# Optimization experiments

Hardware: AMD Instinct MI355X
Metric: run time of the kernel (lower is better)

The kernel has to match this reference:

```python
import jax, jax.numpy as jnp
import numpy as np


def shift_2d(x, H, W):
    # x: (B, T=H*W, C); quarter-channel directional shifts (gamma=1/4), C must be divisible by 4
    B, T, C = x.shape
    g = C // 4
    xi = x.reshape(B, H, W, C)
    # group 0: shift right along W (output[..., 1:, :] = input[..., :-1, :])
    s0 = jnp.pad(xi[:, :, : W - 1, 0:g], ((0, 0), (0, 0), (1, 0), (0, 0)))
    # group 1: shift left along W
    s1 = jnp.pad(xi[:, :, 1:, g : 2 * g], ((0, 0), (0, 0), (0, 1), (0, 0)))
    # group 2: shift down along H
    s2 = jnp.pad(xi[:, : H - 1, :, 2 * g : 3 * g], ((0, 0), (1, 0), (0, 0), (0, 0)))
    # group 3: shift up along H
    s3 = jnp.pad(xi[:, 1:, :, 3 * g : 4 * g], ((0, 0), (0, 1), (0, 0), (0, 0)))
    out = jnp.concatenate([s0, s1, s2, s3], axis=-1)  # C == 4*g here
    return out.reshape(B, T, C)


def wkv(w, u, k, v):
    # RWKV v4 WKV recurrence with running-max numerical stabilization.
    # w, u: (C,) ; k, v: (B, T, C) ; returns y: (B, T, C)
    B, T, C = k.shape
    NEG = jnp.float32(-1e38)

    def step(carry, kv):
        p, q, o = carry  # numerator state, denominator state, running log-max
        kt, vt = kv
        no = jnp.maximum(o, u + kt)
        A = jnp.exp(o - no)
        Bc = jnp.exp(u + kt - no)
        y = (A * p + Bc * vt) / (A * q + Bc)
        no2 = jnp.maximum(w + o, kt)
        A2 = jnp.exp(w + o - no2)
        B2 = jnp.exp(kt - no2)
        return (A2 * p + B2 * vt, A2 * q + B2, no2), y

    init = (jnp.zeros((B, C), k.dtype), jnp.zeros((B, C), k.dtype), jnp.full((B, C), NEG, k.dtype))
    kT = jnp.moveaxis(k, 1, 0)
    vT = jnp.moveaxis(v, 1, 0)
    _, yT = jax.lax.scan(step, init, (kT, vT))
    return jnp.moveaxis(yT, 0, 1)


def setup_inputs() -> dict:
    key = jax.random.key(0)
    ks = jax.random.split(key, 7)
    B, H, W, C = 16, 96, 96, 192
    T = H * W
    x = jax.random.normal(ks[0], (B, T, C), jnp.float32)
    Wk = jax.random.normal(ks[1], (C, C), jnp.float32) * 0.02
    Wv = jax.random.normal(ks[2], (C, C), jnp.float32) * 0.02
    Wr = jax.random.normal(ks[3], (C, C), jnp.float32) * 0.02
    Wo = jax.random.normal(ks[4], (C, C), jnp.float32) * 0.02
    spatial_decay = jax.random.normal(ks[5], (3, C), jnp.float32)
    spatial_first = jax.random.normal(ks[6], (3, C), jnp.float32)
    return {"x": x, "Wk": Wk, "Wv": Wv, "Wr": Wr, "Wo": Wo,
            "spatial_decay": spatial_decay, "spatial_first": spatial_first,
            "H": H, "W": W}


def reference(x, Wk, Wv, Wr, Wo, spatial_decay, spatial_first, H, W):
    B, T, C = x.shape
    xs = shift_2d(x, H, W)
    k = xs @ Wk.T
    v = xs @ Wv.T
    sr = jax.nn.sigmoid(xs @ Wr.T)
    w = spatial_decay[0] / T
    u = spatial_first[0] / T
    y = wkv(w, u, k, v)
    return (sr * y) @ Wo.T
```

## Files before the change

kernel.cpp:

```cpp
#include <hip/hip_runtime.h>
#include <hip/hip_bf16.h>

typedef __bf16 bf16x8 __attribute__((ext_vector_type(8)));
typedef float f32x4 __attribute__((ext_vector_type(4)));

using bf = __hip_bfloat16;

constexpr int cB = 16, cH = 96, cW = 96, cC = 192;
constexpr int cT = cH * cW;
constexpr int cM = cB * cT;
constexpr int CH = 96;
constexpr int NS = cT / CH;
constexpr float Tinv = 1.0f / 9216.0f;

__device__ __forceinline__ int swz(int row, int bytecol) {
    return row * 384 + (bytecol ^ ((row & 7) << 4));
}
__device__ __forceinline__ float bflo(unsigned u) { return __uint_as_float(u << 16); }
__device__ __forceinline__ float bfhi(unsigned u) { return __uint_as_float(u & 0xffff0000u); }

__global__ __launch_bounds__(256) void convw_k(
    const float* __restrict__ Wk, const float* __restrict__ Wv,
    const float* __restrict__ Wr, const float* __restrict__ Wo,
    bf* __restrict__ out)
{
    int i = (blockIdx.x * 256 + threadIdx.x) * 8;
    int mat = i / 36864, off = i % 36864;
    const float* s = mat == 0 ? Wk : (mat == 1 ? Wv : (mat == 2 ? Wr : Wo));
    const float4* sp = reinterpret_cast<const float4*>(s + off);
    float4 a0 = sp[0], a1 = sp[1];
    bf16x8 pk;
    pk[0]=(__bf16)a0.x; pk[1]=(__bf16)a0.y; pk[2]=(__bf16)a0.z; pk[3]=(__bf16)a0.w;
    pk[4]=(__bf16)a1.x; pk[5]=(__bf16)a1.y; pk[6]=(__bf16)a1.z; pk[7]=(__bf16)a1.w;
    *reinterpret_cast<bf16x8*>(reinterpret_cast<__bf16*>(out) + i) = pk;
}

template <int MODE>
__global__ __launch_bounds__(512, 2) void gemm_k(
    const void* __restrict__ Ap, const bf* __restrict__ Wb,
    void* __restrict__ O0, void* __restrict__ O1, void* __restrict__ O2)
{
    constexpr int NMAT = (MODE == 0) ? 3 : 1;
    __shared__ char lds[2 * 64 * 384 + 192 * 384];
    const int tid = threadIdx.x, bx = blockIdx.x;
    const int lane = tid & 63, wid = tid >> 6;
    const int wm = wid >> 2, wn = wid & 3;
    const int lr = lane & 15, lq = lane >> 4;

    int rj[3], kbj[3];
#pragma unroll
    for (int j = 0; j < 3; ++j) { int idx = tid + j * 512; rj[j] = idx / 24; kbj[j] = idx % 24; }

    float4 pf[6];
    int4   pi[3];

    for (int mat = 0; mat < NMAT; ++mat) {
        {
            const bf* Wt = Wb + (size_t)mat * 192 * cC;
            char* Bb = &lds[0] + 2 * 64 * 384;
            for (int it = 0; it < 9; ++it) {
                int idx = tid + it * 512;
                int r = idx / 24, kb = idx % 24;
                int4 val = *reinterpret_cast<const int4*>(Wt + r * cC + kb * 8);
                *reinterpret_cast<int4*>(Bb + swz(r, kb * 16)) = val;
            }
        }
        if constexpr (MODE == 0) {
            const float* Af = (const float*)Ap;
#pragma unroll
            for (int j = 0; j < 3; ++j) {
                int gm = bx * 64 + rj[j];
                int b = gm / cT, t = gm % cT, h = t / cW, w = t % cW;
                int grp = kbj[j] / 6;
                int hs = h + (grp == 2 ? -1 : (grp == 3 ? 1 : 0));
                int ws2 = w + (grp == 0 ? -1 : (grp == 1 ? 1 : 0));
                pf[2*j] = float4{0,0,0,0}; pf[2*j+1] = float4{0,0,0,0};
                if (hs >= 0 && hs < cH && ws2 >= 0 && ws2 < cW) {
                    const float4* s = reinterpret_cast<const float4*>(
                        Af + ((size_t)b * cT + (size_t)hs * cW + ws2) * cC + kbj[j] * 8);
                    pf[2*j] = s[0]; pf[2*j+1] = s[1];
                }
            }
#pragma unroll
            for (int j = 0; j < 3; ++j) {
                bf16x8 pk;
                pk[0]=(__bf16)pf[2*j].x; pk[1]=(__bf16)pf[2*j].y; pk[2]=(__bf16)pf[2*j].z; pk[3]=(__bf16)pf[2*j].w;
                pk[4]=(__bf16)pf[2*j+1].x; pk[5]=(__bf16)pf[2*j+1].y; pk[6]=(__bf16)pf[2*j+1].z; pk[7]=(__bf16)pf[2*j+1].w;
                *reinterpret_cast<bf16x8*>(&lds[0] + swz(rj[j], kbj[j] * 16)) = pk;
            }
        } else {
            const bf* Az = (const bf*)Ap;
#pragma unroll
            for (int j = 0; j < 3; ++j)
                pi[j] = *reinterpret_cast<const int4*>(Az + (size_t)(bx * 64 + rj[j]) * cC + kbj[j] * 8);
#pragma unroll
            for (int j = 0; j < 3; ++j)
                *reinterpret_cast<int4*>(&lds[0] + swz(rj[j], kbj[j] * 16)) = pi[j];
        }
        __syncthreads();

        for (int i = 0; i < 9; ++i) {
            const int tix = bx + 256 * i;
            if (i < 8) {
                const int tn = bx + 256 * (i + 1);
                if constexpr (MODE == 0) {
                    const float* Af = (const float*)Ap;
#pragma unroll
                    for (int j = 0; j < 3; ++j) {
                        int gm = tn * 64 + rj[j];
                        int b = gm / cT, t = gm % cT, h = t / cW, w = t % cW;
                        int grp = kbj[j] / 6;
                        int hs = h + (grp == 2 ? -1 : (grp == 3 ? 1 : 0));
                        int ws2 = w + (grp == 0 ? -1 : (grp == 1 ? 1 : 0));
                        pf[2*j] = float4{0,0,0,0}; pf[2*j+1] = float4{0,0,0,0};
                        if (hs >= 0 && hs < cH && ws2 >= 0 && ws2 < cW) {
                            const float4* s = reinterpret_cast<const float4*>(
                                Af + ((size_t)b * cT + (size_t)hs * cW + ws2) * cC + kbj[j] * 8);
                            pf[2*j] = s[0]; pf[2*j+1] = s[1];
                        }
                    }
                } else {
                    const bf* Az = (const bf*)Ap;
#pragma unroll
                    for (int j = 0; j < 3; ++j)
                        pi[j] = *reinterpret_cast<const int4*>(Az + (size_t)(tn * 64 + rj[j]) * cC + kbj[j] * 8);
                }
            }
            char* Ab = &lds[0] + (i & 1) * (64 * 384);
            char* Bb = &lds[0] + 2 * 64 * 384;
            f32x4 acc[2][3] = {};
#pragma unroll
            for (int kk = 0; kk < 6; ++kk) {
                const int bc = kk * 64 + lq * 16;
                bf16x8 af[2], bfr[3];
#pragma unroll
                for (int mt = 0; mt < 2; ++mt)
                    af[mt] = *reinterpret_cast<const bf16x8*>(Ab + swz(wm * 32 + mt * 16 + lr, bc));
#pragma unroll
                for (int nt = 0; nt < 3; ++nt)
                    bfr[nt] = *reinterpret_cast<const bf16x8*>(Bb + swz(wn * 48 + nt * 16 + lr, bc));
#pragma unroll
                for (int mt = 0; mt < 2; ++mt)
#pragma unroll
                    for (int nt = 0; nt < 3; ++nt)
                        acc[mt][nt] = __builtin_amdgcn_mfma_f32_16x16x32_bf16(
                            af[mt], bfr[nt], acc[mt][nt], 0, 0, 0);
            }
            if constexpr (MODE == 0) {
                bf* Os = (bf*)(mat == 0 ? O0 : (mat == 1 ? O1 : O2));
#pragma unroll
                for (int mt = 0; mt < 2; ++mt)
#pragma unroll
                    for (int nt = 0; nt < 3; ++nt)
#pragma unroll
                        for (int j = 0; j < 4; ++j) {
                            int row = tix * 64 + wm * 32 + mt * 16 + lq * 4 + j;
                            int col = wn * 48 + nt * 16 + lr;
                            float v = acc[mt][nt][j];
                            if (mat == 2) v = 1.0f / (1.0f + __expf(-v));
                            Os[(size_t)row * cC + col] = __float2bfloat16(v);
                        }
            } else {
                float* Os = (float*)O0;
#pragma unroll
                for (int mt = 0; mt < 2; ++mt)
#pragma unroll
                    for (int nt = 0; nt < 3; ++nt)
#pragma unroll
                        for (int j = 0; j < 4; ++j) {
                            int row = tix * 64 + wm * 32 + mt * 16 + lq * 4 + j;
                            int col = wn * 48 + nt * 16 + lr;
                            Os[(size_t)row * cC + col] = acc[mt][nt][j];
                        }
            }
            if (i < 8) {
                char* An = &lds[0] + ((i + 1) & 1) * (64 * 384);
                if constexpr (MODE == 0) {
#pragma unroll
                    for (int j = 0; j < 3; ++j) {
                        bf16x8 pk;
                        pk[0]=(__bf16)pf[2*j].x; pk[1]=(__bf16)pf[2*j].y; pk[2]=(__bf16)pf[2*j].z; pk[3]=(__bf16)pf[2*j].w;
                        pk[4]=(__bf16)pf[2*j+1].x; pk[5]=(__bf16)pf[2*j+1].y; pk[6]=(__bf16)pf[2*j+1].z; pk[7]=(__bf16)pf[2*j+1].w;
                        *reinterpret_cast<bf16x8*>(An + swz(rj[j], kbj[j] * 16)) = pk;
                    }
                } else {
#pragma unroll
                    for (int j = 0; j < 3; ++j)
                        *reinterpret_cast<int4*>(An + swz(rj[j], kbj[j] * 16)) = pi[j];
                }
            }
            __syncthreads();
        }
    }
}

__global__ __launch_bounds__(192) void wkv_pass1(
    const bf* __restrict__ k, const bf* __restrict__ v,
    const float* __restrict__ sd,
    float* __restrict__ stP, float* __restrict__ stQ, float* __restrict__ stO)
{
    const int c2 = threadIdx.x % 96, sub = threadIdx.x / 96;
    const int b = blockIdx.y, ch = blockIdx.x * 2 + sub;
    const int c0 = c2 * 2;
    const float w0 = sd[c0] * Tinv, w1 = sd[c0 + 1] * Tinv;
    size_t base = ((size_t)b * cT + (size_t)ch * CH) * cC + c0;
    float p0 = 0.f, q0 = 0.f, o0 = -1e38f;
    float p1 = 0.f, q1 = 0.f, o1 = -1e38f;
    for (int s = 0; s < CH; ++s) {
        unsigned kw = *reinterpret_cast<const unsigned*>(k + base + (size_t)s * cC);
        unsigned vw = *reinterpret_cast<const unsigned*>(v + base + (size_t)s * cC);
        float kt0 = bflo(kw), kt1 = bfhi(kw);
        float vt0 = bflo(vw), vt1 = bfhi(vw);
        float no0 = fmaxf(w0 + o0, kt0);
        float A0 = __expf(w0 + o0 - no0), B0 = __expf(kt0 - no0);
        p0 = A0 * p0 + B0 * vt0; q0 = A0 * q0 + B0; o0 = no0;
        float no1 = fmaxf(w1 + o1, kt1);
        float A1 = __expf(w1 + o1 - no1), B1 = __expf(kt1 - no1);
        p1 = A1 * p1 + B1 * vt1; q1 = A1 * q1 + B1; o1 = no1;
    }
    size_t si = ((size_t)b * NS + ch) * cC + c0;
    *reinterpret_cast<float2*>(stP + si) = make_float2(p0, p1);
    *reinterpret_cast<float2*>(stQ + si) = make_float2(q0, q1);
    *reinterpret_cast<float2*>(stO + si) = make_float2(o0, o1);
}

__global__ __launch_bounds__(192) void wkv_pass2(
    const float* __restrict__ stP, const float* __restrict__ stQ,
    const float* __restrict__ stO, const float* __restrict__ sd,
    float* __restrict__ iP, float* __restrict__ iQ, float* __restrict__ iO)
{
    const int c = threadIdx.x, b = blockIdx.x;
    const float w = sd[c] * Tinv;
    const float Lw = w * (float)CH;
    float p = 0.f, q = 0.f, o = -1e38f;
    size_t si = (size_t)b * NS * cC + c;
    float sp = stP[si], sq = stQ[si], so = stO[si];
    for (int ch = 0; ch < NS; ++ch) {
        float np_ = 0.f, nq_ = 0.f, no_ = -1e38f;
        if (ch + 1 < NS) {
            size_t sj = si + (size_t)(ch + 1) * cC;
            np_ = stP[sj]; nq_ = stQ[sj]; no_ = stO[sj];
        }
        size_t sc = si + (size_t)ch * cC;
        iP[sc] = p; iQ[sc] = q; iO[sc] = o;
        float po = o + Lw;
        float m = fmaxf(po, so);
        float e1 = __expf(po - m), e2 = __expf(so - m);
        p = e1 * p + e2 * sp;
        q = e1 * q + e2 * sq;
        o = m;
        sp = np_; sq = nq_; so = no_;
    }
}

__global__ __launch_bounds__(192) void wkv_pass3(
    const bf* __restrict__ k, const bf* __restrict__ v, const bf* __restrict__ sr,
    const float* __restrict__ sd, const float* __restrict__ sf,
    const float* __restrict__ iP, const float* __restrict__ iQ,
    const float* __restrict__ iO, bf* __restrict__ z)
{
    const int c2 = threadIdx.x % 96, sub = threadIdx.x / 96;
    const int b = blockIdx.y, ch = blockIdx.x * 2 + sub;
    const int c0 = c2 * 2;
    const float w0 = sd[c0] * Tinv, w1 = sd[c0 + 1] * Tinv;
    const float u0 = sf[c0] * Tinv, u1 = sf[c0 + 1] * Tinv;
    size_t si = ((size_t)b * NS + ch) * cC + c0;
    float2 pp = *reinterpret_cast<const float2*>(iP + si);
    float2 qq = *reinterpret_cast<const float2*>(iQ + si);
    float2 oo = *reinterpret_cast<const float2*>(iO + si);
    float p0 = pp.x, q0 = qq.x, o0 = oo.x;
    float p1 = pp.y, q1 = qq.y, o1 = oo.y;
    size_t base = ((size_t)b * cT + (size_t)ch * CH) * cC + c0;
    for (int s = 0; s < CH; ++s) {
        size_t ix = base + (size_t)s * cC;
        unsigned kw = *reinterpret_cast<const unsigned*>(k + ix);
        unsigned vw = *reinterpret_cast<const unsigned*>(v + ix);
        unsigned rw = *reinterpret_cast<const unsigned*>(sr + ix);
        float kt0 = bflo(kw), kt1 = bfhi(kw);
        float vt0 = bflo(vw), vt1 = bfhi(vw);
        float rt0 = bflo(rw), rt1 = bfhi(rw);

        float no0 = fmaxf(o0, u0 + kt0);
        float Ae0 = __expf(o0 - no0), Be0 = __expf(u0 + kt0 - no0);
        float y0 = (Ae0 * p0 + Be0 * vt0) / (Ae0 * q0 + Be0);
        float no1 = fmaxf(o1, u1 + kt1);
        float Ae1 = __expf(o1 - no1), Be1 = __expf(u1 + kt1 - no1);
        float y1 = (Ae1 * p1 + Be1 * vt1) / (Ae1 * q1 + Be1);

        bf z0 = __float2bfloat16(rt0 * y0);
        bf z1 = __float2bfloat16(rt1 * y1);
        unsigned zp = (unsigned)*reinterpret_cast<unsigned short*>(&z0)
                    | ((unsigned)*reinterpret_cast<unsigned short*>(&z1) << 16);
        *reinterpret_cast<unsigned*>(z + ix) = zp;

        float m0 = fmaxf(w0 + o0, kt0);
        float A0 = __expf(w0 + o0 - m0), B0 = __expf(kt0 - m0);
        p0 = A0 * p0 + B0 * vt0; q0 = A0 * q0 + B0; o0 = m0;
        float m1 = fmaxf(w1 + o1, kt1);
        float A1 = __expf(w1 + o1 - m1), B1 = __expf(kt1 - m1);
        p1 = A1 * p1 + B1 * vt1; q1 = A1 * q1 + B1; o1 = m1;
    }
}

extern "C" void kernel_launch(void* const* d_in, const int* in_sizes, int n_in,
                              void* d_out, int out_size, void* d_ws, size_t ws_size,
                              hipStream_t stream)
{
    const float* x  = (const float*)d_in[0];
    const float* Wk = (const float*)d_in[1];
    const float* Wv = (const float*)d_in[2];
    const float* Wr = (const float*)d_in[3];
    const float* Wo = (const float*)d_in[4];
    const float* sd = (const float*)d_in[5];
    const float* sf = (const float*)d_in[6];
    float* out = (float*)d_out;

    const size_t nEl = (size_t)cM * cC;
    bf* kbuf  = (bf*)d_out;
    bf* srbuf = (bf*)d_out + nEl;
    char* ws = (char*)d_ws;
    bf* vbuf = (bf*)ws;
    bf* zbuf = (bf*)(ws + 2 * nEl);
    const size_t stN = (size_t)cB * NS * cC;
    float* stP = (float*)(ws + 4 * nEl);
    float* stQ = stP + stN;
    float* stO = stQ + stN;
    float* iP  = stO + stN;
    float* iQ  = iP + stN;
    float* iO  = iQ + stN;
    bf* wbf = (bf*)(iO + stN);

    convw_k<<<dim3(72), dim3(256), 0, stream>>>(Wk, Wv, Wr, Wo, wbf);
    gemm_k<0><<<dim3(256), dim3(512), 0, stream>>>(x, wbf, kbuf, vbuf, srbuf);
    wkv_pass1<<<dim3(NS / 2, cB), dim3(192), 0, stream>>>(kbuf, vbuf, sd, stP, stQ, stO);
    wkv_pass2<<<dim3(cB), dim3(192), 0, stream>>>(stP, stQ, stO, sd, iP, iQ, iO);
    wkv_pass3<<<dim3(NS / 2, cB), dim3(192), 0, stream>>>(
        kbuf, vbuf, srbuf, sd, sf, iP, iQ, iO, zbuf);
    gemm_k<1><<<dim3(256), dim3(512), 0, stream>>>(
        zbuf, wbf + (size_t)576 * cC, out, nullptr, nullptr);
}
```

Measured before the change: 245.1 us.

## Halve WKV chunk length, prefetch next-step k/v/r, and scan chunk states in place

Shrinks the per-chunk length of the chunked WKV scan from 96 to 48 steps. This doubles the number of blocks in passes 1 and 3 and shortens each thread's serial dependency chain. Both per-chunk passes now software-prefetch the next timestep's k, v and r words into registers to hide global-load latency behind the exp math. Pass 2 writes the exclusive-prefix states back over the chunk-state buffers instead of separate arrays, which removes three workspace arrays. The trade-off is that the serial pass 2 now loops over twice as many chunks per batch, using only 16 blocks.

```diff
diff --git a/kernel.cpp b/kernel.cpp
--- a/kernel.cpp
+++ b/kernel.cpp
@@ -9,7 +9,7 @@
 constexpr int cB = 16, cH = 96, cW = 96, cC = 192;
 constexpr int cT = cH * cW;
 constexpr int cM = cB * cT;
-constexpr int CH = 96;
+constexpr int CH = 48;
 constexpr int NS = cT / CH;
 constexpr float Tinv = 1.0f / 9216.0f;
 
@@ -206,17 +206,23 @@
     size_t base = ((size_t)b * cT + (size_t)ch * CH) * cC + c0;
     float p0 = 0.f, q0 = 0.f, o0 = -1e38f;
     float p1 = 0.f, q1 = 0.f, o1 = -1e38f;
+    unsigned kwc = *reinterpret_cast<const unsigned*>(k + base);
+    unsigned vwc = *reinterpret_cast<const unsigned*>(v + base);
     for (int s = 0; s < CH; ++s) {
-        unsigned kw = *reinterpret_cast<const unsigned*>(k + base + (size_t)s * cC);
-        unsigned vw = *reinterpret_cast<const unsigned*>(v + base + (size_t)s * cC);
-        float kt0 = bflo(kw), kt1 = bfhi(kw);
-        float vt0 = bflo(vw), vt1 = bfhi(vw);
+        unsigned kwn = 0, vwn = 0;
+        if (s + 1 < CH) {
+            kwn = *reinterpret_cast<const unsigned*>(k + base + (size_t)(s + 1) * cC);
+            vwn = *reinterpret_cast<const unsigned*>(v + base + (size_t)(s + 1) * cC);
+        }
+        float kt0 = bflo(kwc), kt1 = bfhi(kwc);
+        float vt0 = bflo(vwc), vt1 = bfhi(vwc);
         float no0 = fmaxf(w0 + o0, kt0);
         float A0 = __expf(w0 + o0 - no0), B0 = __expf(kt0 - no0);
         p0 = A0 * p0 + B0 * vt0; q0 = A0 * q0 + B0; o0 = no0;
         float no1 = fmaxf(w1 + o1, kt1);
         float A1 = __expf(w1 + o1 - no1), B1 = __expf(kt1 - no1);
         p1 = A1 * p1 + B1 * vt1; q1 = A1 * q1 + B1; o1 = no1;
+        kwc = kwn; vwc = vwn;
     }
     size_t si = ((size_t)b * NS + ch) * cC + c0;
     *reinterpret_cast<float2*>(stP + si) = make_float2(p0, p1);
@@ -225,9 +231,8 @@
 }
 
 __global__ __launch_bounds__(192) void wkv_pass2(
-    const float* __restrict__ stP, const float* __restrict__ stQ,
-    const float* __restrict__ stO, const float* __restrict__ sd,
-    float* __restrict__ iP, float* __restrict__ iQ, float* __restrict__ iO)
+    float* __restrict__ stP, float* __restrict__ stQ, float* __restrict__ stO,
+    const float* __restrict__ sd)
 {
     const int c = threadIdx.x, b = blockIdx.x;
     const float w = sd[c] * Tinv;
@@ -242,7 +247,7 @@
             np_ = stP[sj]; nq_ = stQ[sj]; no_ = stO[sj];
         }
         size_t sc = si + (size_t)ch * cC;
-        iP[sc] = p; iQ[sc] = q; iO[sc] = o;
+        stP[sc] = p; stQ[sc] = q; stO[sc] = o;
         float po = o + Lw;
         float m = fmaxf(po, so);
         float e1 = __expf(po - m), e2 = __expf(so - m);
@@ -271,14 +276,20 @@
     float p0 = pp.x, q0 = qq.x, o0 = oo.x;
     float p1 = pp.y, q1 = qq.y, o1 = oo.y;
     size_t base = ((size_t)b * cT + (size_t)ch * CH) * cC + c0;
+    unsigned kwc = *reinterpret_cast<const unsigned*>(k + base);
+    unsigned vwc = *reinterpret_cast<const unsigned*>(v + base);
+    unsigned rwc = *reinterpret_cast<const unsigned*>(sr + base);
     for (int s = 0; s < CH; ++s) {
-        size_t ix = base + (size_t)s * cC;
-        unsigned kw = *reinterpret_cast<const unsigned*>(k + ix);
-        unsigned vw = *reinterpret_cast<const unsigned*>(v + ix);
-        unsigned rw = *reinterpret_cast<const unsigned*>(sr + ix);
-        float kt0 = bflo(kw), kt1 = bfhi(kw);
-        float vt0 = bflo(vw), vt1 = bfhi(vw);
-        float rt0 = bflo(rw), rt1 = bfhi(rw);
+        unsigned kwn = 0, vwn = 0, rwn = 0;
+        if (s + 1 < CH) {
+            size_t nx = base + (size_t)(s + 1) * cC;
+            kwn = *reinterpret_cast<const unsigned*>(k + nx);
+            vwn = *reinterpret_cast<const unsigned*>(v + nx);
+            rwn = *reinterpret_cast<const unsigned*>(sr + nx);
+        }
+        float kt0 = bflo(kwc), kt1 = bfhi(kwc);
+        float vt0 = bflo(vwc), vt1 = bfhi(vwc);
+        float rt0 = bflo(rwc), rt1 = bfhi(rwc);
 
         float no0 = fmaxf(o0, u0 + kt0);
         float Ae0 = __expf(o0 - no0), Be0 = __expf(u0 + kt0 - no0);
@@ -291,7 +302,7 @@
         bf z1 = __float2bfloat16(rt1 * y1);
         unsigned zp = (unsigned)*reinterpret_cast<unsigned short*>(&z0)
                     | ((unsigned)*reinterpret_cast<unsigned short*>(&z1) << 16);
-        *reinterpret_cast<unsigned*>(z + ix) = zp;
+        *reinterpret_cast<unsigned*>(z + base + (size_t)s * cC) = zp;
 
         float m0 = fmaxf(w0 + o0, kt0);
         float A0 = __expf(w0 + o0 - m0), B0 = __expf(kt0 - m0);
@@ -299,6 +310,7 @@
         float m1 = fmaxf(w1 + o1, kt1);
         float A1 = __expf(w1 + o1 - m1), B1 = __expf(kt1 - m1);
         p1 = A1 * p1 + B1 * vt1; q1 = A1 * q1 + B1; o1 = m1;
+        kwc = kwn; vwc = vwn; rwc = rwn;
     }
 }
 
@@ -325,17 +337,14 @@
     float* stP = (float*)(ws + 4 * nEl);
     float* stQ = stP + stN;
     float* stO = stQ + stN;
-    float* iP  = stO + stN;
-    float* iQ  = iP + stN;
-    float* iO  = iQ + stN;
-    bf* wbf = (bf*)(iO + stN);
+    bf* wbf = (bf*)(stO + stN);
 
     convw_k<<<dim3(72), dim3(256), 0, stream>>>(Wk, Wv, Wr, Wo, wbf);
     gemm_k<0><<<dim3(256), dim3(512), 0, stream>>>(x, wbf, kbuf, vbuf, srbuf);
     wkv_pass1<<<dim3(NS / 2, cB), dim3(192), 0, stream>>>(kbuf, vbuf, sd, stP, stQ, stO);
-    wkv_pass2<<<dim3(cB), dim3(192), 0, stream>>>(stP, stQ, stO, sd, iP, iQ, iO);
+    wkv_pass2<<<dim3(cB), dim3(192), 0, stream>>>(stP, stQ, stO, sd);
     wkv_pass3<<<dim3(NS / 2, cB), dim3(192), 0, stream>>>(
-        kbuf, vbuf, srbuf, sd, sf, iP, iQ, iO, zbuf);
+        kbuf, vbuf, srbuf, sd, sf, stP, stQ, stO, zbuf);
     gemm_k<1><<<dim3(256), dim3(512), 0, stream>>>(
         zbuf, wbf + (size_t)576 * cC, out, nullptr, nullptr);
 }
```

Measured after the change: 236.4 us. 1.04x faster.
